# Kernel tuning notes

Measured on AMD Instinct MI355X. Metric: run time of the kernel, lower is better.

The kernel has to match this reference:

```python
import jax, jax.numpy as jnp
import numpy as np

ALPHA = 0.5        # damping from conf['alpha']
MAX_ITERS = 30     # fixed-point iterations (conf uses up to 150 with eps early-exit)
GN_GROUPS = 3
GN_EPS = 1e-5
SLOPE = 0.01       # F.leaky_relu default negative_slope


def _conv(x, w, b, pad):
    y = jax.lax.conv_general_dilated(
        x, w, window_strides=(1, 1), padding=[(pad, pad), (pad, pad)],
        dimension_numbers=("NCHW", "OIHW", "NCHW"))
    return y + b[None, :, None, None]


def _leaky(x):
    return jnp.where(x >= 0, x, SLOPE * x)


def _groupnorm(x, gamma, beta):
    N, C, H, W = x.shape
    xg = x.reshape(N, GN_GROUPS, C // GN_GROUPS, H, W)
    mu = xg.mean(axis=(2, 3, 4), keepdims=True)
    var = xg.var(axis=(2, 3, 4), keepdims=True)
    xg = (xg - mu) * jax.lax.rsqrt(var + GN_EPS)
    x = xg.reshape(N, C, H, W)
    return x * gamma[None, :, None, None] + beta[None, :, None, None]


def setup_inputs() -> dict:
    key = jax.random.key(0)
    ks = jax.random.split(key, 8)
    image = jax.random.normal(ks[0], (1024, 3, 32, 32), dtype=jnp.float32)
    # Unit params (small init keeps the fixed-point iteration contractive)
    w1 = jax.random.normal(ks[1], (6, 8, 5, 5), dtype=jnp.float32) * 0.05
    b1 = jnp.zeros((6,), jnp.float32)
    gamma = jnp.ones((6,), jnp.float32)
    beta = jnp.zeros((6,), jnp.float32)
    w2 = jax.random.normal(ks[2], (5, 6, 5, 5), dtype=jnp.float32) * 0.05
    b2 = jnp.zeros((5,), jnp.float32)
    # detection head: Conv2d(5, 10, 32, padding=0) -> full-image conv
    wh = jax.random.normal(ks[3], (10, 5, 32, 32), dtype=jnp.float32) * 0.01
    bh = jnp.zeros((10,), jnp.float32)
    return {"image": image, "w1": w1, "b1": b1, "gamma": gamma, "beta": beta,
            "w2": w2, "b2": b2, "wh": wh, "bh": bh}


def reference(image, w1, b1, gamma, beta, w2, b2, wh, bh):
    N = image.shape[0]
    z0 = jnp.zeros((N, 5, 32, 32), image.dtype)

    def unit(z):
        zx = jnp.concatenate([z, image], axis=1)
        h = _groupnorm(_leaky(_conv(zx, w1, b1, 2)), gamma, beta)
        return _leaky(_conv(h, w2, b2, 2))

    def step(z, _):
        z = (1.0 - ALPHA) * z + ALPHA * unit(z)
        return z, None

    z, _ = jax.lax.scan(step, z0, None, length=MAX_ITERS)
    return _conv(z, wh, bh, 0)
```

## Files before the change

kernel.cpp:

```cpp
#include <hip/hip_runtime.h>
#include <hip/hip_fp16.h>


typedef _Float16 half8 __attribute__((ext_vector_type(8)));
typedef float f32x4 __attribute__((ext_vector_type(4)));

#define HOFF  34
#define NBUF  (71 * 36 * 4)

__device__ __forceinline__ unsigned pk2(float a, float b) {
    __half2 h = __float22half2_rn(make_float2(a, b));
    return *reinterpret_cast<unsigned*>(&h);
}
__device__ __forceinline__ float2 up2(unsigned u) {
    __half2 h = *reinterpret_cast<__half2*>(&u);
    return __half22float2(h);
}
__device__ __forceinline__ float lrelu(float x) { return fmaxf(x, 0.01f * x); }
__device__ __forceinline__ int bofs(int r, int x) {
    return ((r * 36 + x) * 16) ^ ((x & 8) << 1);
}

__global__ void pack_weights(const float* __restrict__ w1,
                             const float* __restrict__ w2,
                             unsigned* __restrict__ ws)
{
    int t = blockIdx.x * 256 + threadIdx.x;
    if (t < 640) {
        int c = t >> 6, l = t & 63;
        int row = l & 15, tg = l >> 4;
        int dx = row >> 3, oc = row & 7;
        int ty = c >> 1, tx = 4 * (c & 1) + tg, kx = tx - dx;
        unsigned q[4];
        #pragma unroll
        for (int d = 0; d < 4; ++d) {
            float v0 = 0.f, v1 = 0.f;
            if (oc < 6 && kx >= 0 && kx < 5) {
                v0 = w1[(oc * 8 + 2 * d) * 25 + ty * 5 + kx];
                v1 = w1[(oc * 8 + 2 * d + 1) * 25 + ty * 5 + kx];
            }
            q[d] = pk2(v0, v1);
        }
        *(uint4*)&ws[t * 4] = make_uint4(q[0], q[1], q[2], q[3]);
    } else if (t < 1280) {
        int u = t - 640;
        int c = u >> 6, l = u & 63;
        int row = l & 15, tg = l >> 4;
        int dx = row >> 3, oc = row & 7;
        int ty = c >> 1, tx = 4 * (c & 1) + tg, kx = tx - dx;
        unsigned q[4];
        #pragma unroll
        for (int d = 0; d < 4; ++d) {
            float v0 = 0.f, v1 = 0.f;
            if (oc < 5 && kx >= 0 && kx < 5) {
                if (2 * d < 6)     v0 = w2[(oc * 6 + 2 * d) * 25 + ty * 5 + kx];
                if (2 * d + 1 < 6) v1 = w2[(oc * 6 + 2 * d + 1) * 25 + ty * 5 + kx];
            }
            q[d] = pk2(v0, v1);
        }
        *(uint4*)&ws[2560 + u * 4] = make_uint4(q[0], q[1], q[2], q[3]);
    }
}

__global__ __launch_bounds__(256, 1)
void deq_kernel(const float* __restrict__ image,
                const unsigned* __restrict__ wks,
                const float* __restrict__ b1,
                const float* __restrict__ gam, const float* __restrict__ bet,
                const float* __restrict__ b2,
                const float* __restrict__ wh, const float* __restrict__ bh,
                float* __restrict__ out)
{
    __shared__ __align__(16) unsigned buf[NBUF];
    __shared__ float red[48];

    const int n    = blockIdx.x;
    const int tid  = threadIdx.x;
    const int lane = tid & 63;
    const int wid  = tid >> 6;
    const int col  = lane & 15;
    const int tg   = lane >> 4;
    const int dxl  = tg >> 1;
    const int sub  = tg & 1;

    for (int p = tid; p < NBUF; p += 256) buf[p] = 0u;
    __syncthreads();

    {
        const int yy = tid >> 3, xx0 = (tid & 7) << 2;
        float4 i0 = *(const float4*)&image[(n * 3 + 0) * 1024 + yy * 32 + xx0];
        float4 i1 = *(const float4*)&image[(n * 3 + 1) * 1024 + yy * 32 + xx0];
        float4 i2 = *(const float4*)&image[(n * 3 + 2) * 1024 + yy * 32 + xx0];
        float a0[4] = {i0.x, i0.y, i0.z, i0.w};
        float a1[4] = {i1.x, i1.y, i1.z, i1.w};
        float a2[4] = {i2.x, i2.y, i2.z, i2.w};
        #pragma unroll
        for (int i = 0; i < 4; ++i) {
            unsigned* bp = (unsigned*)((char*)buf + bofs(yy + 2, xx0 + 2 + i));
            bp[2] = pk2(0.f, a0[i]);
            bp[3] = pk2(a1[i], a2[i]);
        }
    }

    uint4 f1[10], f2[10];
    #pragma unroll
    for (int c = 0; c < 10; ++c) {
        f1[c] = *(const uint4*)&wks[(c * 64 + lane) * 4];
        f2[c] = *(const uint4*)&wks[2560 + (c * 64 + lane) * 4];
    }

    int sx2[2];
    #pragma unroll
    for (int txh = 0; txh < 2; ++txh) {
        int x = 2 * col + 4 * txh + tg;
        sx2[txh] = (x * 16) ^ ((x & 8) << 1);
    }

    const int chb = (tg & 1) * 4;
    float b1q[4], b2q[4], gq[4], bq[4];
    #pragma unroll
    for (int r = 0; r < 4; ++r) {
        int oc = chb + r;
        b1q[r] = (oc < 6) ? b1[oc] : 0.f;
        b2q[r] = (oc < 5) ? b2[oc] : 0.f;
        gq[r]  = (oc < 6) ? gam[oc] : 0.f;
        bq[r]  = (oc < 6) ? bet[oc] : 0.f;
    }
    const f32x4 ai1 = {b1q[0], b1q[1], b1q[2], b1q[3]};
    const f32x4 ai2 = {b2q[0], b2q[1], b2q[2], b2q[3]};

    __syncthreads();

    const char* zb = (const char*)buf;
    const int ay0 = wid << 3;
    const int hwp0 = bofs(0, 2 * col + dxl + 2) + sub * 8;

    #pragma unroll 1
    for (int it = 0; it < 30; ++it) {
        f32x4 acc[8];
        #pragma unroll
        for (int g = 0; g < 8; ++g) acc[g] = ai1;

        #pragma unroll
        for (int pr = 0; pr < 12; ++pr) {
            const char* rowp = zb + (ay0 + pr) * 576;
            #pragma unroll
            for (int txh = 0; txh < 2; ++txh) {
                half8 pv = *(const half8*)(rowp + sx2[txh]);
                #pragma unroll
                for (int ty = 0; ty < 5; ++ty) {
                    const int g = pr - ty;
                    if (g >= 0 && g < 8)
                        acc[g] = __builtin_amdgcn_mfma_f32_16x16x32_f16(
                            __builtin_bit_cast(half8, f1[ty * 2 + txh]), pv, acc[g], 0, 0, 0);
                }
            }
        }

        float ps_lo = 0.f, ps_hi = 0.f, pq_lo = 0.f, pq_hi = 0.f;
        #pragma unroll
        for (int g = 0; g < 8; ++g) {
            float h0 = lrelu(acc[g][0]), h1 = lrelu(acc[g][1]);
            float h2 = lrelu(acc[g][2]), h3 = lrelu(acc[g][3]);
            acc[g][0] = h0; acc[g][1] = h1; acc[g][2] = h2; acc[g][3] = h3;
            ps_lo += h0 + h1;  pq_lo = fmaf(h0, h0, fmaf(h1, h1, pq_lo));
            ps_hi += h2 + h3;  pq_hi = fmaf(h2, h2, fmaf(h3, h3, pq_hi));
        }

        #pragma unroll
        for (int m = 1; m <= 8; m <<= 1) {
            ps_lo += __shfl_xor(ps_lo, m); ps_hi += __shfl_xor(ps_hi, m);
            pq_lo += __shfl_xor(pq_lo, m); pq_hi += __shfl_xor(pq_hi, m);
        }
        ps_lo += __shfl_xor(ps_lo, 32); ps_hi += __shfl_xor(ps_hi, 32);
        pq_lo += __shfl_xor(pq_lo, 32); pq_hi += __shfl_xor(pq_hi, 32);
        if (lane == 0)  { red[wid * 8 + 0] = ps_lo; red[wid * 8 + 1] = ps_hi;
                          red[wid * 8 + 4] = pq_lo; red[wid * 8 + 5] = pq_hi; }
        if (lane == 16) { red[wid * 8 + 2] = ps_lo; red[wid * 8 + 6] = pq_lo; }
        __syncthreads();

        float invm[3], meanm[3];
        #pragma unroll
        for (int g3 = 0; g3 < 3; ++g3) {
            float s = 0.f, q = 0.f;
            #pragma unroll
            for (int w = 0; w < 4; ++w) { s += red[w * 8 + g3]; q += red[w * 8 + 4 + g3]; }
            float mean = s * (1.f / 2048.f);
            float var  = q * (1.f / 2048.f) - mean * mean;
            invm[g3]  = rsqrtf(var + 1e-5f);
            meanm[g3] = mean;
        }
        float scq[4], shq[4];
        #pragma unroll
        for (int r = 0; r < 4; ++r) {
            int oc = chb + r;
            float inv  = (oc < 6) ? invm[oc >> 1]  : 0.f;
            float mean = (oc < 6) ? meanm[oc >> 1] : 0.f;
            scq[r] = inv * gq[r];
            shq[r] = bq[r] - mean * scq[r];
        }

        #pragma unroll
        for (int g = 0; g < 8; ++g) {
            float h0 = fmaf(acc[g][0], scq[0], shq[0]);
            float h1 = fmaf(acc[g][1], scq[1], shq[1]);
            float h2 = fmaf(acc[g][2], scq[2], shq[2]);
            float h3 = fmaf(acc[g][3], scq[3], shq[3]);
            char* wp = (char*)buf + (ay0 + g + 2 + HOFF) * 576 + hwp0;
            *(uint2*)wp = make_uint2(pk2(h0, h1), pk2(h2, h3));
        }
        __syncthreads();

        #pragma unroll
        for (int g = 0; g < 8; ++g) acc[g] = ai2;

        #pragma unroll
        for (int pr = 0; pr < 12; ++pr) {
            const char* rowp = zb + (HOFF + ay0 + pr) * 576;
            #pragma unroll
            for (int txh = 0; txh < 2; ++txh) {
                half8 pv = *(const half8*)(rowp + sx2[txh]);
                #pragma unroll
                for (int ty = 0; ty < 5; ++ty) {
                    const int g = pr - ty;
                    if (g >= 0 && g < 8)
                        acc[g] = __builtin_amdgcn_mfma_f32_16x16x32_f16(
                            __builtin_bit_cast(half8, f2[ty * 2 + txh]), pv, acc[g], 0, 0, 0);
                }
            }
        }

        #pragma unroll
        for (int g = 0; g < 8; ++g) {
            char* zp = (char*)buf + bofs(ay0 + g + 2, 2 * col + dxl + 2);
            if (sub == 0) {
                uint2 zo = *(uint2*)zp;
                float2 za = up2(zo.x), zc = up2(zo.y);
                float z0 = 0.5f * za.x + 0.5f * lrelu(acc[g][0]);
                float z1 = 0.5f * za.y + 0.5f * lrelu(acc[g][1]);
                float z2 = 0.5f * zc.x + 0.5f * lrelu(acc[g][2]);
                float z3 = 0.5f * zc.y + 0.5f * lrelu(acc[g][3]);
                *(uint2*)zp = make_uint2(pk2(z0, z1), pk2(z2, z3));
            } else {
                _Float16* pz = (_Float16*)(zp + 8);
                float z4 = 0.5f * (float)pz[0] + 0.5f * lrelu(acc[g][0]);
                pz[0] = (_Float16)z4;
            }
        }
        __syncthreads();
    }

    {
        const int yy = tid >> 3, xx0 = (tid & 7) << 2;
        float zf[5][4];
        #pragma unroll
        for (int i = 0; i < 4; ++i) {
            const unsigned* bp = (const unsigned*)((const char*)buf + bofs(yy + 2, xx0 + 2 + i));
            float2 f0 = up2(bp[0]), fb = up2(bp[1]), fc = up2(bp[2]);
            zf[0][i] = f0.x; zf[1][i] = f0.y; zf[2][i] = fb.x; zf[3][i] = fb.y; zf[4][i] = fc.x;
        }
        float ho[10];
        #pragma unroll
        for (int o = 0; o < 10; ++o) ho[o] = 0.f;
        #pragma unroll
        for (int c = 0; c < 5; ++c) {
            #pragma unroll
            for (int o = 0; o < 10; ++o) {
                float4 wv = *(const float4*)&wh[(o * 5 + c) * 1024 + yy * 32 + xx0];
                ho[o] = fmaf(zf[c][0], wv.x, ho[o]);
                ho[o] = fmaf(zf[c][1], wv.y, ho[o]);
                ho[o] = fmaf(zf[c][2], wv.z, ho[o]);
                ho[o] = fmaf(zf[c][3], wv.w, ho[o]);
            }
        }
        #pragma unroll
        for (int m = 1; m < 64; m <<= 1) {
            #pragma unroll
            for (int o = 0; o < 10; ++o) ho[o] += __shfl_xor(ho[o], m);
        }
        if (lane == 0) {
            #pragma unroll
            for (int o = 0; o < 10; ++o) red[wid * 10 + o] = ho[o];
        }
    }
    __syncthreads();
    if (tid < 10)
        out[n * 10 + tid] = red[tid] + red[10 + tid] + red[20 + tid] + red[30 + tid] + bh[tid];
}

extern "C" void kernel_launch(void* const* d_in, const int* in_sizes, int n_in,
                              void* d_out, int out_size, void* d_ws, size_t ws_size,
                              hipStream_t stream) {
    const float* image = (const float*)d_in[0];
    const float* w1    = (const float*)d_in[1];
    const float* b1    = (const float*)d_in[2];
    const float* gam   = (const float*)d_in[3];
    const float* bet   = (const float*)d_in[4];
    const float* w2    = (const float*)d_in[5];
    const float* b2    = (const float*)d_in[6];
    const float* wh    = (const float*)d_in[7];
    const float* bh    = (const float*)d_in[8];
    float* out = (float*)d_out;
    unsigned* ws = (unsigned*)d_ws;

    pack_weights<<<5, 256, 0, stream>>>(w1, w2, ws);

    const int N = in_sizes[0] / (3 * 32 * 32);
    deq_kernel<<<N, 256, 0, stream>>>(image, ws, b1, gam, bet, b2, wh, bh, out);
}
```

Baseline: 309.6 us.

## Process two images per block with interleaved MFMA streams

Each workgroup now runs the fixed-point iteration for two images at once, with separate LDS buffers and reductions. MFMAs for both images share the same weight fragments and are interleaved to raise instruction-level parallelism. Barriers and weight loads are amortized over two images. This doubles accumulator registers and LDS per block and halves the grid, which may reduce occupancy or cause spills, and it assumes N is even.

```diff
diff --git a/kernel.cpp b/kernel.cpp
--- a/kernel.cpp
+++ b/kernel.cpp
@@ -71,10 +71,12 @@
                 const float* __restrict__ wh, const float* __restrict__ bh,
                 float* __restrict__ out)
 {
-    __shared__ __align__(16) unsigned buf[NBUF];
-    __shared__ float red[48];
-
-    const int n    = blockIdx.x;
+    __shared__ __align__(16) unsigned bufA[NBUF];
+    __shared__ __align__(16) unsigned bufB[NBUF];
+    __shared__ float redA[48], redB[48];
+
+    const int n0   = blockIdx.x * 2;
+    const int n1   = n0 + 1;
     const int tid  = threadIdx.x;
     const int lane = tid & 63;
     const int wid  = tid >> 6;
@@ -83,22 +85,27 @@
     const int dxl  = tg >> 1;
     const int sub  = tg & 1;
 
-    for (int p = tid; p < NBUF; p += 256) buf[p] = 0u;
+    for (int p = tid; p < NBUF; p += 256) { bufA[p] = 0u; bufB[p] = 0u; }
     __syncthreads();
 
     {
         const int yy = tid >> 3, xx0 = (tid & 7) << 2;
-        float4 i0 = *(const float4*)&image[(n * 3 + 0) * 1024 + yy * 32 + xx0];
-        float4 i1 = *(const float4*)&image[(n * 3 + 1) * 1024 + yy * 32 + xx0];
-        float4 i2 = *(const float4*)&image[(n * 3 + 2) * 1024 + yy * 32 + xx0];
-        float a0[4] = {i0.x, i0.y, i0.z, i0.w};
-        float a1[4] = {i1.x, i1.y, i1.z, i1.w};
-        float a2[4] = {i2.x, i2.y, i2.z, i2.w};
-        #pragma unroll
-        for (int i = 0; i < 4; ++i) {
-            unsigned* bp = (unsigned*)((char*)buf + bofs(yy + 2, xx0 + 2 + i));
-            bp[2] = pk2(0.f, a0[i]);
-            bp[3] = pk2(a1[i], a2[i]);
+        #pragma unroll
+        for (int im = 0; im < 2; ++im) {
+            const int nn = n0 + im;
+            unsigned* bb = im ? bufB : bufA;
+            float4 i0 = *(const float4*)&image[(nn * 3 + 0) * 1024 + yy * 32 + xx0];
+            float4 i1 = *(const float4*)&image[(nn * 3 + 1) * 1024 + yy * 32 + xx0];
+            float4 i2 = *(const float4*)&image[(nn * 3 + 2) * 1024 + yy * 32 + xx0];
+            float a0[4] = {i0.x, i0.y, i0.z, i0.w};
+            float a1[4] = {i1.x, i1.y, i1.z, i1.w};
+            float a2[4] = {i2.x, i2.y, i2.z, i2.w};
+            #pragma unroll
+            for (int i = 0; i < 4; ++i) {
+                unsigned* bp = (unsigned*)((char*)bb + bofs(yy + 2, xx0 + 2 + i));
+                bp[2] = pk2(0.f, a0[i]);
+                bp[3] = pk2(a1[i], a2[i]);
+            }
         }
     }
 
@@ -131,120 +138,182 @@
 
     __syncthreads();
 
-    const char* zb = (const char*)buf;
     const int ay0 = wid << 3;
     const int hwp0 = bofs(0, 2 * col + dxl + 2) + sub * 8;
 
     #pragma unroll 1
     for (int it = 0; it < 30; ++it) {
-        f32x4 acc[8];
-        #pragma unroll
-        for (int g = 0; g < 8; ++g) acc[g] = ai1;
+        f32x4 accA[8], accB[8];
+        #pragma unroll
+        for (int g = 0; g < 8; ++g) { accA[g] = ai1; accB[g] = ai1; }
 
         #pragma unroll
         for (int pr = 0; pr < 12; ++pr) {
-            const char* rowp = zb + (ay0 + pr) * 576;
+            const char* rpA = (const char*)bufA + (ay0 + pr) * 576;
+            const char* rpB = (const char*)bufB + (ay0 + pr) * 576;
             #pragma unroll
             for (int txh = 0; txh < 2; ++txh) {
-                half8 pv = *(const half8*)(rowp + sx2[txh]);
+                half8 pvA = *(const half8*)(rpA + sx2[txh]);
+                half8 pvB = *(const half8*)(rpB + sx2[txh]);
                 #pragma unroll
                 for (int ty = 0; ty < 5; ++ty) {
                     const int g = pr - ty;
-                    if (g >= 0 && g < 8)
-                        acc[g] = __builtin_amdgcn_mfma_f32_16x16x32_f16(
-                            __builtin_bit_cast(half8, f1[ty * 2 + txh]), pv, acc[g], 0, 0, 0);
+                    if (g >= 0 && g < 8) {
+                        half8 wf = __builtin_bit_cast(half8, f1[ty * 2 + txh]);
+                        accA[g] = __builtin_amdgcn_mfma_f32_16x16x32_f16(wf, pvA, accA[g], 0, 0, 0);
+                        accB[g] = __builtin_amdgcn_mfma_f32_16x16x32_f16(wf, pvB, accB[g], 0, 0, 0);
+                    }
                 }
             }
         }
 
-        float ps_lo = 0.f, ps_hi = 0.f, pq_lo = 0.f, pq_hi = 0.f;
+        float psA_lo = 0.f, psA_hi = 0.f, pqA_lo = 0.f, pqA_hi = 0.f;
+        float psB_lo = 0.f, psB_hi = 0.f, pqB_lo = 0.f, pqB_hi = 0.f;
         #pragma unroll
         for (int g = 0; g < 8; ++g) {
-            float h0 = lrelu(acc[g][0]), h1 = lrelu(acc[g][1]);
-            float h2 = lrelu(acc[g][2]), h3 = lrelu(acc[g][3]);
-            acc[g][0] = h0; acc[g][1] = h1; acc[g][2] = h2; acc[g][3] = h3;
-            ps_lo += h0 + h1;  pq_lo = fmaf(h0, h0, fmaf(h1, h1, pq_lo));
-            ps_hi += h2 + h3;  pq_hi = fmaf(h2, h2, fmaf(h3, h3, pq_hi));
+            float a0 = lrelu(accA[g][0]), a1 = lrelu(accA[g][1]);
+            float a2 = lrelu(accA[g][2]), a3 = lrelu(accA[g][3]);
+            accA[g][0] = a0; accA[g][1] = a1; accA[g][2] = a2; accA[g][3] = a3;
+            psA_lo += a0 + a1;  pqA_lo = fmaf(a0, a0, fmaf(a1, a1, pqA_lo));
+            psA_hi += a2 + a3;  pqA_hi = fmaf(a2, a2, fmaf(a3, a3, pqA_hi));
+            float c0 = lrelu(accB[g][0]), c1 = lrelu(accB[g][1]);
+            float c2 = lrelu(accB[g][2]), c3 = lrelu(accB[g][3]);
+            accB[g][0] = c0; accB[g][1] = c1; accB[g][2] = c2; accB[g][3] = c3;
+            psB_lo += c0 + c1;  pqB_lo = fmaf(c0, c0, fmaf(c1, c1, pqB_lo));
+            psB_hi += c2 + c3;  pqB_hi = fmaf(c2, c2, fmaf(c3, c3, pqB_hi));
         }
 
         #pragma unroll
         for (int m = 1; m <= 8; m <<= 1) {
-            ps_lo += __shfl_xor(ps_lo, m); ps_hi += __shfl_xor(ps_hi, m);
-            pq_lo += __shfl_xor(pq_lo, m); pq_hi += __shfl_xor(pq_hi, m);
-        }
-        ps_lo += __shfl_xor(ps_lo, 32); ps_hi += __shfl_xor(ps_hi, 32);
-        pq_lo += __shfl_xor(pq_lo, 32); pq_hi += __shfl_xor(pq_hi, 32);
-        if (lane == 0)  { red[wid * 8 + 0] = ps_lo; red[wid * 8 + 1] = ps_hi;
-                          red[wid * 8 + 4] = pq_lo; red[wid * 8 + 5] = pq_hi; }
-        if (lane == 16) { red[wid * 8 + 2] = ps_lo; red[wid * 8 + 6] = pq_lo; }
+            psA_lo += __shfl_xor(psA_lo, m); psA_hi += __shfl_xor(psA_hi, m);
+            pqA_lo += __shfl_xor(pqA_lo, m); pqA_hi += __shfl_xor(pqA_hi, m);
+            psB_lo += __shfl_xor(psB_lo, m); psB_hi += __shfl_xor(psB_hi, m);
+            pqB_lo += __shfl_xor(pqB_lo, m); pqB_hi += __shfl_xor(pqB_hi, m);
+        }
+        psA_lo += __shfl_xor(psA_lo, 32); psA_hi += __shfl_xor(psA_hi, 32);
+        pqA_lo += __shfl_xor(pqA_lo, 32); pqA_hi += __shfl_xor(pqA_hi, 32);
+        psB_lo += __shfl_xor(psB_lo, 32); psB_hi += __shfl_xor(psB_hi, 32);
+        pqB_lo += __shfl_xor(pqB_lo, 32); pqB_hi += __shfl_xor(pqB_hi, 32);
+        if (lane == 0) {
+            redA[wid * 8 + 0] = psA_lo; redA[wid * 8 + 1] = psA_hi;
+            redA[wid * 8 + 4] = pqA_lo; redA[wid * 8 + 5] = pqA_hi;
+            redB[wid * 8 + 0] = psB_lo; redB[wid * 8 + 1] = psB_hi;
+            redB[wid * 8 + 4] = pqB_lo; redB[wid * 8 + 5] = pqB_hi;
+        }
+        if (lane == 16) {
+            redA[wid * 8 + 2] = psA_lo; redA[wid * 8 + 6] = pqA_lo;
+            redB[wid * 8 + 2] = psB_lo; redB[wid * 8 + 6] = pqB_lo;
+        }
         __syncthreads();
 
-        float invm[3], meanm[3];
-        #pragma unroll
-        for (int g3 = 0; g3 < 3; ++g3) {
-            float s = 0.f, q = 0.f;
-            #pragma unroll
-            for (int w = 0; w < 4; ++w) { s += red[w * 8 + g3]; q += red[w * 8 + 4 + g3]; }
-            float mean = s * (1.f / 2048.f);
-            float var  = q * (1.f / 2048.f) - mean * mean;
-            invm[g3]  = rsqrtf(var + 1e-5f);
-            meanm[g3] = mean;
-        }
-        float scq[4], shq[4];
-        #pragma unroll
-        for (int r = 0; r < 4; ++r) {
-            int oc = chb + r;
-            float inv  = (oc < 6) ? invm[oc >> 1]  : 0.f;
-            float mean = (oc < 6) ? meanm[oc >> 1] : 0.f;
-            scq[r] = inv * gq[r];
-            shq[r] = bq[r] - mean * scq[r];
+        float scqA[4], shqA[4], scqB[4], shqB[4];
+        {
+            float invm[3], meanm[3];
+            #pragma unroll
+            for (int g3 = 0; g3 < 3; ++g3) {
+                float s = 0.f, q = 0.f;
+                #pragma unroll
+                for (int w = 0; w < 4; ++w) { s += redA[w * 8 + g3]; q += redA[w * 8 + 4 + g3]; }
+                float mean = s * (1.f / 2048.f);
+                float var  = q * (1.f / 2048.f) - mean * mean;
+                invm[g3]  = rsqrtf(var + 1e-5f);
+                meanm[g3] = mean;
+            }
+            #pragma unroll
+            for (int r = 0; r < 4; ++r) {
+                int oc = chb + r;
+                float inv  = (oc < 6) ? invm[oc >> 1]  : 0.f;
+                float mean = (oc < 6) ? meanm[oc >> 1] : 0.f;
+                scqA[r] = inv * gq[r];
+                shqA[r] = bq[r] - mean * scqA[r];
+            }
+        }
+        {
+            float invm[3], meanm[3];
+            #pragma unroll
+            for (int g3 = 0; g3 < 3; ++g3) {
+                float s = 0.f, q = 0.f;
+                #pragma unroll
+                for (int w = 0; w < 4; ++w) { s += redB[w * 8 + g3]; q += redB[w * 8 + 4 + g3]; }
+                float mean = s * (1.f / 2048.f);
+                float var  = q * (1.f / 2048.f) - mean * mean;
+                invm[g3]  = rsqrtf(var + 1e-5f);
+                meanm[g3] = mean;
+            }
+            #pragma unroll
+            for (int r = 0; r < 4; ++r) {
+                int oc = chb + r;
+                float inv  = (oc < 6) ? invm[oc >> 1]  : 0.f;
+                float mean = (oc < 6) ? meanm[oc >> 1] : 0.f;
+                scqB[r] = inv * gq[r];
+                shqB[r] = bq[r] - mean * scqB[r];
+            }
         }
 
         #pragma unroll
         for (int g = 0; g < 8; ++g) {
-            float h0 = fmaf(acc[g][0], scq[0], shq[0]);
-            float h1 = fmaf(acc[g][1], scq[1], shq[1]);
-            float h2 = fmaf(acc[g][2], scq[2], shq[2]);
-            float h3 = fmaf(acc[g][3], scq[3], shq[3]);
-            char* wp = (char*)buf + (ay0 + g + 2 + HOFF) * 576 + hwp0;
-            *(uint2*)wp = make_uint2(pk2(h0, h1), pk2(h2, h3));
+            float h0 = fmaf(accA[g][0], scqA[0], shqA[0]);
+            float h1 = fmaf(accA[g][1], scqA[1], shqA[1]);
+            float h2 = fmaf(accA[g][2], scqA[2], shqA[2]);
+            float h3 = fmaf(accA[g][3], scqA[3], shqA[3]);
+            char* wpA = (char*)bufA + (ay0 + g + 2 + HOFF) * 576 + hwp0;
+            *(uint2*)wpA = make_uint2(pk2(h0, h1), pk2(h2, h3));
+            float k0 = fmaf(accB[g][0], scqB[0], shqB[0]);
+            float k1 = fmaf(accB[g][1], scqB[1], shqB[1]);
+            float k2 = fmaf(accB[g][2], scqB[2], shqB[2]);
+            float k3 = fmaf(accB[g][3], scqB[3], shqB[3]);
+            char* wpB = (char*)bufB + (ay0 + g + 2 + HOFF) * 576 + hwp0;
+            *(uint2*)wpB = make_uint2(pk2(k0, k1), pk2(k2, k3));
         }
         __syncthreads();
 
         #pragma unroll
-        for (int g = 0; g < 8; ++g) acc[g] = ai2;
+        for (int g = 0; g < 8; ++g) { accA[g] = ai2; accB[g] = ai2; }
 
         #pragma unroll
         for (int pr = 0; pr < 12; ++pr) {
-            const char* rowp = zb + (HOFF + ay0 + pr) * 576;
+            const char* rpA = (const char*)bufA + (HOFF + ay0 + pr) * 576;
+            const char* rpB = (const char*)bufB + (HOFF + ay0 + pr) * 576;
             #pragma unroll
             for (int txh = 0; txh < 2; ++txh) {
-                half8 pv = *(const half8*)(rowp + sx2[txh]);
+                half8 pvA = *(const half8*)(rpA + sx2[txh]);
+                half8 pvB = *(const half8*)(rpB + sx2[txh]);
                 #pragma unroll
                 for (int ty = 0; ty < 5; ++ty) {
                     const int g = pr - ty;
-                    if (g >= 0 && g < 8)
-                        acc[g] = __builtin_amdgcn_mfma_f32_16x16x32_f16(
-                            __builtin_bit_cast(half8, f2[ty * 2 + txh]), pv, acc[g], 0, 0, 0);
+                    if (g >= 0 && g < 8) {
+                        half8 wf = __builtin_bit_cast(half8, f2[ty * 2 + txh]);
+                        accA[g] = __builtin_amdgcn_mfma_f32_16x16x32_f16(wf, pvA, accA[g], 0, 0, 0);
+                        accB[g] = __builtin_amdgcn_mfma_f32_16x16x32_f16(wf, pvB, accB[g], 0, 0, 0);
+                    }
                 }
             }
         }
 
         #pragma unroll
         for (int g = 0; g < 8; ++g) {
-            char* zp = (char*)buf + bofs(ay0 + g + 2, 2 * col + dxl + 2);
+            char* zpA = (char*)bufA + bofs(ay0 + g + 2, 2 * col + dxl + 2);
+            char* zpB = (char*)bufB + bofs(ay0 + g + 2, 2 * col + dxl + 2);
             if (sub == 0) {
-                uint2 zo = *(uint2*)zp;
-                float2 za = up2(zo.x), zc = up2(zo.y);
-                float z0 = 0.5f * za.x + 0.5f * lrelu(acc[g][0]);
-                float z1 = 0.5f * za.y + 0.5f * lrelu(acc[g][1]);
-                float z2 = 0.5f * zc.x + 0.5f * lrelu(acc[g][2]);
-                float z3 = 0.5f * zc.y + 0.5f * lrelu(acc[g][3]);
-                *(uint2*)zp = make_uint2(pk2(z0, z1), pk2(z2, z3));
+                uint2 za = *(uint2*)zpA;
+                float2 a0 = up2(za.x), a1 = up2(za.y);
+                *(uint2*)zpA = make_uint2(
+                    pk2(0.5f * a0.x + 0.5f * lrelu(accA[g][0]),
+                        0.5f * a0.y + 0.5f * lrelu(accA[g][1])),
+                    pk2(0.5f * a1.x + 0.5f * lrelu(accA[g][2]),
+                        0.5f * a1.y + 0.5f * lrelu(accA[g][3])));
+                uint2 zb = *(uint2*)zpB;
+                float2 c0 = up2(zb.x), c1 = up2(zb.y);
+                *(uint2*)zpB = make_uint2(
+                    pk2(0.5f * c0.x + 0.5f * lrelu(accB[g][0]),
+                        0.5f * c0.y + 0.5f * lrelu(accB[g][1])),
+                    pk2(0.5f * c1.x + 0.5f * lrelu(accB[g][2]),
+                        0.5f * c1.y + 0.5f * lrelu(accB[g][3])));
             } else {
-                _Float16* pz = (_Float16*)(zp + 8);
-                float z4 = 0.5f * (float)pz[0] + 0.5f * lrelu(acc[g][0]);
-                pz[0] = (_Float16)z4;
+                _Float16* pa = (_Float16*)(zpA + 8);
+                pa[0] = (_Float16)(0.5f * (float)pa[0] + 0.5f * lrelu(accA[g][0]));
+                _Float16* pb = (_Float16*)(zpB + 8);
+                pb[0] = (_Float16)(0.5f * (float)pb[0] + 0.5f * lrelu(accB[g][0]));
             }
         }
         __syncthreads();
@@ -252,40 +321,47 @@
 
     {
         const int yy = tid >> 3, xx0 = (tid & 7) << 2;
-        float zf[5][4];
-        #pragma unroll
-        for (int i = 0; i < 4; ++i) {
-            const unsigned* bp = (const unsigned*)((const char*)buf + bofs(yy + 2, xx0 + 2 + i));
-            float2 f0 = up2(bp[0]), fb = up2(bp[1]), fc = up2(bp[2]);
-            zf[0][i] = f0.x; zf[1][i] = f0.y; zf[2][i] = fb.x; zf[3][i] = fb.y; zf[4][i] = fc.x;
-        }
-        float ho[10];
-        #pragma unroll
-        for (int o = 0; o < 10; ++o) ho[o] = 0.f;
-        #pragma unroll
-        for (int c = 0; c < 5; ++c) {
-            #pragma unroll
-            for (int o = 0; o < 10; ++o) {
-                float4 wv = *(const float4*)&wh[(o * 5 + c) * 1024 + yy * 32 + xx0];
-                ho[o] = fmaf(zf[c][0], wv.x, ho[o]);
-                ho[o] = fmaf(zf[c][1], wv.y, ho[o]);
-                ho[o] = fmaf(zf[c][2], wv.z, ho[o]);
-                ho[o] = fmaf(zf[c][3], wv.w, ho[o]);
-            }
-        }
-        #pragma unroll
-        for (int m = 1; m < 64; m <<= 1) {
-            #pragma unroll
-            for (int o = 0; o < 10; ++o) ho[o] += __shfl_xor(ho[o], m);
-        }
-        if (lane == 0) {
-            #pragma unroll
-            for (int o = 0; o < 10; ++o) red[wid * 10 + o] = ho[o];
+        #pragma unroll 1
+        for (int im = 0; im < 2; ++im) {
+            const unsigned* bb = im ? bufB : bufA;
+            float zf[5][4];
+            #pragma unroll
+            for (int i = 0; i < 4; ++i) {
+                const unsigned* bp = (const unsigned*)((const char*)bb + bofs(yy + 2, xx0 + 2 + i));
+                float2 f0 = up2(bp[0]), fb = up2(bp[1]), fc = up2(bp[2]);
+                zf[0][i] = f0.x; zf[1][i] = f0.y; zf[2][i] = fb.x; zf[3][i] = fb.y; zf[4][i] = fc.x;
+            }
+            float ho[10];
+            #pragma unroll
+            for (int o = 0; o < 10; ++o) ho[o] = 0.f;
+            #pragma unroll
+            for (int c = 0; c < 5; ++c) {
+                #pragma unroll
+                for (int o = 0; o < 10; ++o) {
+                    float4 wv = *(const float4*)&wh[(o * 5 + c) * 1024 + yy * 32 + xx0];
+                    ho[o] = fmaf(zf[c][0], wv.x, ho[o]);
+                    ho[o] = fmaf(zf[c][1], wv.y, ho[o]);
+                    ho[o] = fmaf(zf[c][2], wv.z, ho[o]);
+                    ho[o] = fmaf(zf[c][3], wv.w, ho[o]);
+                }
+            }
+            #pragma unroll
+            for (int m = 1; m < 64; m <<= 1) {
+                #pragma unroll
+                for (int o = 0; o < 10; ++o) ho[o] += __shfl_xor(ho[o], m);
+            }
+            float* rr = im ? redB : redA;
+            if (lane == 0) {
+                #pragma unroll
+                for (int o = 0; o < 10; ++o) rr[wid * 10 + o] = ho[o];
+            }
         }
     }
     __syncthreads();
-    if (tid < 10)
-        out[n * 10 + tid] = red[tid] + red[10 + tid] + red[20 + tid] + red[30 + tid] + bh[tid];
+    if (tid < 10) {
+        out[n0 * 10 + tid] = redA[tid] + redA[10 + tid] + redA[20 + tid] + redA[30 + tid] + bh[tid];
+        out[n1 * 10 + tid] = redB[tid] + redB[10 + tid] + redB[20 + tid] + redB[30 + tid] + bh[tid];
+    }
 }
 
 extern "C" void kernel_launch(void* const* d_in, const int* in_sizes, int n_in,
@@ -306,5 +382,5 @@
     pack_weights<<<5, 256, 0, stream>>>(w1, w2, ws);
 
     const int N = in_sizes[0] / (3 * 32 * 32);
-    deq_kernel<<<N, 256, 0, stream>>>(image, ws, b1, gam, bet, b2, wh, bh, out);
-}
+    deq_kernel<<<N / 2, 256, 0, stream>>>(image, ws, b1, gam, bet, b2, wh, bh, out);
+}
```

Measured after the change: 489.3 us. 58.0% more time.

## Fold GroupNorm affine into conv2 weights and move weight fragments to LDS

Applied to the files above, without the earlier changes.

Conv weight fragments now live in LDS and are reloaded into registers each iteration instead of being held in registers, and the launch bound rises to two blocks per CU to raise occupancy. GroupNorm scale is folded into the conv2 weights with half-precision multiplies. The shift is folded into an extra constant-one input channel stored in the padded hidden buffer. This removes the separate normalize pass and one barrier per iteration, and unnormalized activations are written straight to LDS. The cost is extra per-iteration LDS traffic and weight rescaling, plus fp16 rounding of the scaled weights, which could change accuracy.

```diff
diff --git a/kernel.cpp b/kernel.cpp
--- a/kernel.cpp
+++ b/kernel.cpp
@@ -5,8 +5,11 @@
 typedef _Float16 half8 __attribute__((ext_vector_type(8)));
 typedef float f32x4 __attribute__((ext_vector_type(4)));
 
-#define HOFF  34
-#define NBUF  (71 * 36 * 4)
+#define HOFF   34
+#define NBUF   (71 * 36 * 4)
+#define WL1_DW 10224
+#define WL2_DW 12784
+#define NLDS   15344
 
 __device__ __forceinline__ unsigned pk2(float a, float b) {
     __half2 h = __float22half2_rn(make_float2(a, b));
@@ -16,10 +19,13 @@
     __half2 h = *reinterpret_cast<__half2*>(&u);
     return __half22float2(h);
 }
+__device__ __forceinline__ unsigned hmul2(unsigned a, unsigned b) {
+    __half2 r = __hmul2(*reinterpret_cast<__half2*>(&a), *reinterpret_cast<__half2*>(&b));
+    return *reinterpret_cast<unsigned*>(&r);
+}
 __device__ __forceinline__ float lrelu(float x) { return fmaxf(x, 0.01f * x); }
-__device__ __forceinline__ int bofs(int r, int x) {
-    return ((r * 36 + x) * 16) ^ ((x & 8) << 1);
-}
+__device__ __forceinline__ int swz(int x) { return (x * 16) ^ ((x & 8) << 1); }
+__device__ __forceinline__ int bofs(int r, int x) { return r * 576 + swz(x); }
 
 __global__ void pack_weights(const float* __restrict__ w1,
                              const float* __restrict__ w2,
@@ -62,7 +68,7 @@
     }
 }
 
-__global__ __launch_bounds__(256, 1)
+__global__ __launch_bounds__(256, 2)
 void deq_kernel(const float* __restrict__ image,
                 const unsigned* __restrict__ wks,
                 const float* __restrict__ b1,
@@ -71,7 +77,7 @@
                 const float* __restrict__ wh, const float* __restrict__ bh,
                 float* __restrict__ out)
 {
-    __shared__ __align__(16) unsigned buf[NBUF];
+    __shared__ __align__(16) unsigned lds[NLDS];
     __shared__ float red[48];
 
     const int n    = blockIdx.x;
@@ -83,7 +89,11 @@
     const int dxl  = tg >> 1;
     const int sub  = tg & 1;
 
-    for (int p = tid; p < NBUF; p += 256) buf[p] = 0u;
+    for (int p = tid; p < NBUF; p += 256) lds[p] = 0u;
+    for (int p = tid; p < 2560; p += 256) {
+        lds[WL1_DW + p] = wks[p];
+        lds[WL2_DW + p] = wks[2560 + p];
+    }
     __syncthreads();
 
     {
@@ -96,54 +106,49 @@
         float a2[4] = {i2.x, i2.y, i2.z, i2.w};
         #pragma unroll
         for (int i = 0; i < 4; ++i) {
-            unsigned* bp = (unsigned*)((char*)buf + bofs(yy + 2, xx0 + 2 + i));
+            unsigned* bp = (unsigned*)((char*)lds + bofs(yy + 2, xx0 + 2 + i));
             bp[2] = pk2(0.f, a0[i]);
             bp[3] = pk2(a1[i], a2[i]);
-        }
-    }
-
-    uint4 f1[10], f2[10];
-    #pragma unroll
-    for (int c = 0; c < 10; ++c) {
-        f1[c] = *(const uint4*)&wks[(c * 64 + lane) * 4];
-        f2[c] = *(const uint4*)&wks[2560 + (c * 64 + lane) * 4];
+            unsigned* hp = (unsigned*)((char*)lds + bofs(yy + 2 + HOFF, xx0 + 2 + i));
+            hp[3] = 0x00003C00u;
+        }
     }
 
     int sx2[2];
     #pragma unroll
-    for (int txh = 0; txh < 2; ++txh) {
-        int x = 2 * col + 4 * txh + tg;
-        sx2[txh] = (x * 16) ^ ((x & 8) << 1);
-    }
-
-    const int chb = (tg & 1) * 4;
-    float b1q[4], b2q[4], gq[4], bq[4];
+    for (int txh = 0; txh < 2; ++txh)
+        sx2[txh] = swz(2 * col + 4 * txh + tg);
+
+    float b1q[4], b2q[4];
     #pragma unroll
     for (int r = 0; r < 4; ++r) {
-        int oc = chb + r;
+        int oc = (tg * 4 + r) & 7;
         b1q[r] = (oc < 6) ? b1[oc] : 0.f;
         b2q[r] = (oc < 5) ? b2[oc] : 0.f;
-        gq[r]  = (oc < 6) ? gam[oc] : 0.f;
-        bq[r]  = (oc < 6) ? bet[oc] : 0.f;
     }
     const f32x4 ai1 = {b1q[0], b1q[1], b1q[2], b1q[3]};
     const f32x4 ai2 = {b2q[0], b2q[1], b2q[2], b2q[3]};
 
     __syncthreads();
 
-    const char* zb = (const char*)buf;
     const int ay0 = wid << 3;
-    const int hwp0 = bofs(0, 2 * col + dxl + 2) + sub * 8;
+    const int hwB = bofs(0, 2 * col + dxl + 2);
+    const int wlo = lane << 2;
 
     #pragma unroll 1
     for (int it = 0; it < 30; ++it) {
+        uint4 fw[10];
+        #pragma unroll
+        for (int c = 0; c < 10; ++c)
+            fw[c] = *(const uint4*)&lds[WL1_DW + c * 256 + wlo];
+
         f32x4 acc[8];
         #pragma unroll
         for (int g = 0; g < 8; ++g) acc[g] = ai1;
 
         #pragma unroll
         for (int pr = 0; pr < 12; ++pr) {
-            const char* rowp = zb + (ay0 + pr) * 576;
+            const char* rowp = (const char*)lds + (ay0 + pr) * 576;
             #pragma unroll
             for (int txh = 0; txh < 2; ++txh) {
                 half8 pv = *(const half8*)(rowp + sx2[txh]);
@@ -152,7 +157,7 @@
                     const int g = pr - ty;
                     if (g >= 0 && g < 8)
                         acc[g] = __builtin_amdgcn_mfma_f32_16x16x32_f16(
-                            __builtin_bit_cast(half8, f1[ty * 2 + txh]), pv, acc[g], 0, 0, 0);
+                            __builtin_bit_cast(half8, fw[ty * 2 + txh]), pv, acc[g], 0, 0, 0);
                 }
             }
         }
@@ -162,9 +167,15 @@
         for (int g = 0; g < 8; ++g) {
             float h0 = lrelu(acc[g][0]), h1 = lrelu(acc[g][1]);
             float h2 = lrelu(acc[g][2]), h3 = lrelu(acc[g][3]);
-            acc[g][0] = h0; acc[g][1] = h1; acc[g][2] = h2; acc[g][3] = h3;
             ps_lo += h0 + h1;  pq_lo = fmaf(h0, h0, fmaf(h1, h1, pq_lo));
             ps_hi += h2 + h3;  pq_hi = fmaf(h2, h2, fmaf(h3, h3, pq_hi));
+            char* wp = (char*)lds + (ay0 + g + 2 + HOFF) * 576 + (hwB - 0 * 576);
+            wp = (char*)lds + bofs(ay0 + g + 2 + HOFF, 2 * col + dxl + 2);
+            if (sub == 0) {
+                *(uint2*)wp = make_uint2(pk2(h0, h1), pk2(h2, h3));
+            } else {
+                *(unsigned*)(wp + 8) = pk2(h0, h1);
+            }
         }
 
         #pragma unroll
@@ -179,7 +190,7 @@
         if (lane == 16) { red[wid * 8 + 2] = ps_lo; red[wid * 8 + 6] = pq_lo; }
         __syncthreads();
 
-        float invm[3], meanm[3];
+        float scv[6], shv[6];
         #pragma unroll
         for (int g3 = 0; g3 < 3; ++g3) {
             float s = 0.f, q = 0.f;
@@ -187,36 +198,35 @@
             for (int w = 0; w < 4; ++w) { s += red[w * 8 + g3]; q += red[w * 8 + 4 + g3]; }
             float mean = s * (1.f / 2048.f);
             float var  = q * (1.f / 2048.f) - mean * mean;
-            invm[g3]  = rsqrtf(var + 1e-5f);
-            meanm[g3] = mean;
-        }
-        float scq[4], shq[4];
-        #pragma unroll
-        for (int r = 0; r < 4; ++r) {
-            int oc = chb + r;
-            float inv  = (oc < 6) ? invm[oc >> 1]  : 0.f;
-            float mean = (oc < 6) ? meanm[oc >> 1] : 0.f;
-            scq[r] = inv * gq[r];
-            shq[r] = bq[r] - mean * scq[r];
-        }
-
-        #pragma unroll
-        for (int g = 0; g < 8; ++g) {
-            float h0 = fmaf(acc[g][0], scq[0], shq[0]);
-            float h1 = fmaf(acc[g][1], scq[1], shq[1]);
-            float h2 = fmaf(acc[g][2], scq[2], shq[2]);
-            float h3 = fmaf(acc[g][3], scq[3], shq[3]);
-            char* wp = (char*)buf + (ay0 + g + 2 + HOFF) * 576 + hwp0;
-            *(uint2*)wp = make_uint2(pk2(h0, h1), pk2(h2, h3));
-        }
-        __syncthreads();
+            float inv  = rsqrtf(var + 1e-5f);
+            #pragma unroll
+            for (int k = 0; k < 2; ++k) {
+                int c = 2 * g3 + k;
+                scv[c] = inv * gam[c];
+                shv[c] = bet[c] - mean * scv[c];
+            }
+        }
+        unsigned sp0 = pk2(scv[0], scv[1]), sp1 = pk2(scv[2], scv[3]), sp2 = pk2(scv[4], scv[5]);
+
+        #pragma unroll
+        for (int c = 0; c < 10; ++c) {
+            uint4 wr = *(const uint4*)&lds[WL2_DW + c * 256 + wlo];
+            float2 a = up2(wr.x), b = up2(wr.y), cc = up2(wr.z);
+            float pw = fmaf(a.x, shv[0], fmaf(a.y, shv[1],
+                       fmaf(b.x, shv[2], fmaf(b.y, shv[3],
+                       fmaf(cc.x, shv[4], cc.y * shv[5])))));
+            fw[c].x = hmul2(wr.x, sp0);
+            fw[c].y = hmul2(wr.y, sp1);
+            fw[c].z = hmul2(wr.z, sp2);
+            fw[c].w = pk2(pw, 0.f);
+        }
 
         #pragma unroll
         for (int g = 0; g < 8; ++g) acc[g] = ai2;
 
         #pragma unroll
         for (int pr = 0; pr < 12; ++pr) {
-            const char* rowp = zb + (HOFF + ay0 + pr) * 576;
+            const char* rowp = (const char*)lds + (HOFF + ay0 + pr) * 576;
             #pragma unroll
             for (int txh = 0; txh < 2; ++txh) {
                 half8 pv = *(const half8*)(rowp + sx2[txh]);
@@ -225,14 +235,14 @@
                     const int g = pr - ty;
                     if (g >= 0 && g < 8)
                         acc[g] = __builtin_amdgcn_mfma_f32_16x16x32_f16(
-                            __builtin_bit_cast(half8, f2[ty * 2 + txh]), pv, acc[g], 0, 0, 0);
+                            __builtin_bit_cast(half8, fw[ty * 2 + txh]), pv, acc[g], 0, 0, 0);
                 }
             }
         }
 
         #pragma unroll
         for (int g = 0; g < 8; ++g) {
-            char* zp = (char*)buf + bofs(ay0 + g + 2, 2 * col + dxl + 2);
+            char* zp = (char*)lds + bofs(ay0 + g + 2, 2 * col + dxl + 2);
             if (sub == 0) {
                 uint2 zo = *(uint2*)zp;
                 float2 za = up2(zo.x), zc = up2(zo.y);
@@ -255,7 +265,7 @@
         float zf[5][4];
         #pragma unroll
         for (int i = 0; i < 4; ++i) {
-            const unsigned* bp = (const unsigned*)((const char*)buf + bofs(yy + 2, xx0 + 2 + i));
+            const unsigned* bp = (const unsigned*)((const char*)lds + bofs(yy + 2, xx0 + 2 + i));
             float2 f0 = up2(bp[0]), fb = up2(bp[1]), fc = up2(bp[2]);
             zf[0][i] = f0.x; zf[1][i] = f0.y; zf[2][i] = fb.x; zf[3][i] = fb.y; zf[4][i] = fc.x;
         }
```

After: 335.8 us. 1.08x slower.
